# Performance work log

Hardware: AMD Instinct MI355X
Metric: run time of the kernel (lower is better)

## Reference

```python
import jax, jax.numpy as jnp
import numpy as np


def _grad(x, axis):
    """torch.gradient with unit spacing: central diff interior, one-sided edges."""
    def sl(a, b):
        idx = [slice(None)] * x.ndim
        idx[axis] = slice(a, b)
        return x[tuple(idx)]
    left = sl(1, 2) - sl(0, 1)                 # (x[1]-x[0])
    mid = (sl(2, None) - sl(0, -2)) * 0.5      # (x[i+1]-x[i-1])/2
    right = sl(-1, None) - sl(-2, -1)          # (x[-1]-x[-2])
    return jnp.concatenate([left, mid, right], axis=axis)


def _mse0(e):
    return jnp.mean(e * e)  # MSE against zeros


def _phy_loss(V_all, P_all, F_all, Re):
    Vy = V_all[:, :, :, :, 0, :]
    Vx = V_all[:, :, :, :, 1, :]
    Vz = V_all[:, :, :, :, 2, :]
    Fy = F_all[:, :, :, :, 0, :]
    Fx = F_all[:, :, :, :, 1, :]
    Fz = F_all[:, :, :, :, 2, :]
    # first derivatives (dims: 1=y, 2=x, 3=z, 4=t)
    dVydt, dVydy, dVydx, dVydz = _grad(Vy, 4), _grad(Vy, 1), _grad(Vy, 2), _grad(Vy, 3)
    dVxdt, dVxdy, dVxdx, dVxdz = _grad(Vx, 4), _grad(Vx, 1), _grad(Vx, 2), _grad(Vx, 3)
    dVzdt, dVzdy, dVzdx, dVzdz = _grad(Vz, 4), _grad(Vz, 1), _grad(Vz, 2), _grad(Vz, 3)
    dPdx, dPdy, dPdz = _grad(P_all, 2), _grad(P_all, 1), _grad(P_all, 3)
    # second derivatives
    lapVx = _grad(dVxdx, 2) + _grad(dVxdy, 1) + _grad(dVxdz, 3)
    lapVy = _grad(dVydx, 2) + _grad(dVydy, 1) + _grad(dVydz, 3)
    lapVz = _grad(dVzdx, 2) + _grad(dVzdy, 1) + _grad(dVzdz, 3)
    e1 = dVydt + (Vx * dVydx + Vy * dVydy + Vz * dVydz + dPdy) - Re * lapVy + Fy
    e2 = dVxdt + (Vx * dVxdx + Vy * dVxdy + Vz * dVxdz + dPdx) - Re * lapVx + Fx
    e3 = dVzdt + (Vx * dVzdx + Vy * dVzdy + Vz * dVzdz + dPdz) - Re * lapVz + Fz
    e4 = dVxdx + dVydy + dVzdz
    return _mse0(e1) + _mse0(e2) + _mse0(e3) + _mse0(e4)


def _time_loss(C_all, Y_data, X_last):
    Y_last = jnp.concatenate([X_last, Y_data[:, :, :, :, :-1]], axis=4)
    t1 = jnp.mean((Y_last - Y_data) ** 2)
    t2 = jnp.mean((C_all - Y_data) ** 2)
    return jnp.where(jax.lax.stop_gradient(t1) < jax.lax.stop_gradient(t2), t2 - t1, 0.0)


def setup_inputs() -> dict:
    key = jax.random.key(0)
    ks = jax.random.split(key, 9)
    B, S, T = 2, 48, 16
    f = jnp.float32
    return {
        "C_all": jax.random.normal(ks[0], (B, S, S, S, T), f),
        "V_all": jax.random.normal(ks[1], (B, S, S, S, 3, T), f),
        "P_all": jax.random.normal(ks[2], (B, S, S, S, T), f),
        "X_all": jax.random.normal(ks[3], (B, S, S, S, T), f),
        "X1_all": jax.random.normal(ks[4], (B, S, S, S, T), f),
        "F_all": jax.random.normal(ks[5], (B, S, S, S, 3, T), f),
        "Re": jnp.ones((1,), f),
        "X_last": jax.random.normal(ks[6], (B, S, S, S, 1), f),
        "Y_data": jax.random.normal(ks[7], (B, S, S, S, T), f),
        "maskd0": jnp.ones((1,), f),
        "maskd1": jnp.ones((1,), f),
        "maskd2": jnp.ones((1,), f),
    }


def reference(C_all, V_all, P_all, X_all, X1_all, F_all, Re, X_last, Y_data, maskd0, maskd1, maskd2):
    main1 = jnp.mean((X1_all - Y_data) ** 2)
    main2 = jnp.mean((X_all - Y_data) ** 2)
    phy = _phy_loss(V_all, P_all, F_all, Re)
    tl = _time_loss(C_all, Y_data, X_last)
    return (main1, main2, phy, tl)
```

## Files before the change

### kernel.cpp

```cpp
#include <hip/hip_runtime.h>

#define S 48
#define T 16
#define NTOT (2 * S * S * S * T)
#define NBLK (2 * S * S)
#define NSLOT 64

using f4 = __attribute__((ext_vector_type(4))) float;

__device__ __forceinline__ float d1(const float* __restrict__ fc, int i, int N, int stride) {
    int dl = (i > 0) ? -stride : 0;
    int dr = (i < N - 1) ? stride : 0;
    float w = (i > 0 && i < N - 1) ? 0.5f : 1.0f;
    return (fc[dr] - fc[dl]) * w;
}

__device__ __forceinline__ float d2c(const float* __restrict__ fc, int i, int N, int stride) {
    int j0, j1, j2;
    float c0, c1, c2;
    if (i == 0)          { j0 = 0;  j1 = 1;  j2 = 2; c0 = 0.5f;  c1 = -1.0f;  c2 = 0.5f;  }
    else if (i == 1)     { j0 = -1; j1 = 0;  j2 = 2; c0 = 0.5f;  c1 = -0.75f; c2 = 0.25f; }
    else if (i == N - 1) { j0 = -2; j1 = -1; j2 = 0; c0 = 0.5f;  c1 = -1.0f;  c2 = 0.5f;  }
    else if (i == N - 2) { j0 = -2; j1 = 0;  j2 = 1; c0 = 0.25f; c1 = -0.75f; c2 = 0.5f;  }
    else                 { j0 = -2; j1 = 0;  j2 = 2; c0 = 0.25f; c1 = -0.5f;  c2 = 0.25f; }
    return c0 * fc[j0 * stride] + c1 * fc[j1 * stride] + c2 * fc[j2 * stride];
}

__device__ __forceinline__ float d2c_i(const float* __restrict__ fc, float center, int stride) {
    return 0.25f * (fc[-2 * stride] + fc[2 * stride]) - 0.5f * center;
}

__global__ __launch_bounds__(256) void fused_loss(
    const float* __restrict__ Cmat, const float* __restrict__ V,
    const float* __restrict__ P, const float* __restrict__ Xa,
    const float* __restrict__ X1a, const float* __restrict__ F,
    const float* __restrict__ Rep, const float* __restrict__ Xlast,
    const float* __restrict__ Y, float* __restrict__ ws)
{
    const int bidx = blockIdx.x;
    const int x = bidx % S;
    const int y = (bidx / S) % S;
    const int b = bidx / (S * S);
    const int sp0 = ((b * S + y) * S + x) * S;
    const int n0 = sp0 * T;
    const int v0 = sp0 * 48;

    __shared__ float sV[3][S][T];
    __shared__ float sP[S][T];
    __shared__ float sY[S][T];

    const int tid = threadIdx.x;

    for (int j = tid; j < 5 * 192; j += 256) {
        const int a  = j / 192;
        const int r  = j % 192;
        const int z  = r >> 2;
        const int t4 = (r & 3) << 2;
        const float* src;
        float* dst;
        if (a < 3)       { src = V + v0 + z * 48 + a * 16 + t4; dst = &sV[a][z][t4]; }
        else if (a == 3) { src = P + n0 + z * 16 + t4;          dst = &sP[z][t4]; }
        else             { src = Y + n0 + z * 16 + t4;          dst = &sY[z][t4]; }
        *reinterpret_cast<f4*>(dst) = *reinterpret_cast<const f4*>(src);
    }
    __syncthreads();

    const float re = Rep[0];
    const bool xint = (x >= 2 && x < S - 2);
    const bool yint = (y >= 2 && y < S - 2);

    float am1 = 0.f, am2 = 0.f, aphy = 0.f, at1 = 0.f, at2 = 0.f;

    #pragma unroll 1
    for (int i = tid; i < S * T; i += 256) {
        const int z = i >> 4;
        const int t = i & 15;
        const int n = n0 + i;
        const int vb = v0 + z * 48 + t;

        const float yv  = sY[z][t];
        const float dm1 = X1a[n] - yv;
        const float dm2 = Xa[n] - yv;
        am1 += dm1 * dm1;
        am2 += dm2 * dm2;
        const float yprev = (t == 0) ? Xlast[sp0 + z] : sY[z][t - 1];
        const float dt1 = yprev - yv;
        const float dt2 = Cmat[n] - yv;
        at1 += dt1 * dt1;
        at2 += dt2 * dt2;

        const float vy = sV[0][z][t], vx = sV[1][z][t], vz = sV[2][z][t];
        float div;

        {
            const float* c = &sV[0][z][t];
            const float ddt = d1(c, t, T, 1);
            const float ddz = d1(c, z, S, T);
            const float lz  = d2c(c, z, S, T);
            const float* g = V + vb;
            const float ddx = d1(g, x, S, 2304);
            const float ddy = d1(g, y, S, 110592);
            const float lx = xint ? d2c_i(g, vy, 2304)   : d2c(g, x, S, 2304);
            const float ly = yint ? d2c_i(g, vy, 110592) : d2c(g, y, S, 110592);
            const float dPdy = d1(P + n, y, S, 36864);
            const float e1 = ddt + (vx * ddx + vy * ddy + vz * ddz + dPdy)
                             - re * (lz + lx + ly) + F[vb];
            aphy += e1 * e1;
            div = ddy;
        }
        {
            const float* c = &sV[1][z][t];
            const float ddt = d1(c, t, T, 1);
            const float ddz = d1(c, z, S, T);
            const float lz  = d2c(c, z, S, T);
            const float* g = V + vb + 16;
            const float ddx = d1(g, x, S, 2304);
            const float ddy = d1(g, y, S, 110592);
            const float lx = xint ? d2c_i(g, vx, 2304)   : d2c(g, x, S, 2304);
            const float ly = yint ? d2c_i(g, vx, 110592) : d2c(g, y, S, 110592);
            const float dPdx = d1(P + n, x, S, 768);
            const float e2 = ddt + (vx * ddx + vy * ddy + vz * ddz + dPdx)
                             - re * (lz + lx + ly) + F[vb + 16];
            aphy += e2 * e2;
            div += ddx;
        }
        {
            const float* c = &sV[2][z][t];
            const float ddt = d1(c, t, T, 1);
            const float ddz = d1(c, z, S, T);
            const float lz  = d2c(c, z, S, T);
            const float* g = V + vb + 32;
            const float ddx = d1(g, x, S, 2304);
            const float ddy = d1(g, y, S, 110592);
            const float lx = xint ? d2c_i(g, vz, 2304)   : d2c(g, x, S, 2304);
            const float ly = yint ? d2c_i(g, vz, 110592) : d2c(g, y, S, 110592);
            const float dPdz = d1(&sP[z][t], z, S, T);
            const float e3 = ddt + (vx * ddx + vy * ddy + vz * ddz + dPdz)
                             - re * (lz + lx + ly) + F[vb + 32];
            aphy += e3 * e3;
            div += ddz;
            aphy += div * div;
        }
    }

    #pragma unroll
    for (int off = 32; off > 0; off >>= 1) {
        am1  += __shfl_down(am1, off);
        am2  += __shfl_down(am2, off);
        aphy += __shfl_down(aphy, off);
        at1  += __shfl_down(at1, off);
        at2  += __shfl_down(at2, off);
    }
    __shared__ float sred[4][5];
    const int lane = tid & 63;
    const int wv   = tid >> 6;
    if (lane == 0) {
        sred[wv][0] = am1; sred[wv][1] = am2; sred[wv][2] = aphy;
        sred[wv][3] = at1; sred[wv][4] = at2;
    }
    __syncthreads();
    if (tid == 0) {
        float s0 = 0.f, s1 = 0.f, s2 = 0.f, s3 = 0.f, s4 = 0.f;
        #pragma unroll
        for (int w = 0; w < 4; ++w) {
            s0 += sred[w][0]; s1 += sred[w][1]; s2 += sred[w][2];
            s3 += sred[w][3]; s4 += sred[w][4];
        }
        float* slot = ws + (bidx & (NSLOT - 1)) * 16;
        atomicAdd(&slot[0], s0);
        atomicAdd(&slot[1], s1);
        atomicAdd(&slot[2], s2);
        atomicAdd(&slot[3], s3);
        atomicAdd(&slot[4], s4);
    }
}

__global__ void finalize_kernel(const float* __restrict__ ws, float* __restrict__ out) {
    const int l = threadIdx.x;
    float s0 = ws[l * 16 + 0];
    float s1 = ws[l * 16 + 1];
    float s2 = ws[l * 16 + 2];
    float s3 = ws[l * 16 + 3];
    float s4 = ws[l * 16 + 4];
    #pragma unroll
    for (int off = 32; off > 0; off >>= 1) {
        s0 += __shfl_down(s0, off);
        s1 += __shfl_down(s1, off);
        s2 += __shfl_down(s2, off);
        s3 += __shfl_down(s3, off);
        s4 += __shfl_down(s4, off);
    }
    if (l == 0) {
        const float invN = 1.0f / (float)NTOT;
        const float m1  = s0 * invN;
        const float m2  = s1 * invN;
        const float phy = s2 * invN;
        const float t1  = s3 * invN;
        const float t2  = s4 * invN;
        out[0] = m1;
        out[1] = m2;
        out[2] = phy;
        out[3] = (t1 < t2) ? (t2 - t1) : 0.0f;
    }
}

extern "C" void kernel_launch(void* const* d_in, const int* in_sizes, int n_in,
                              void* d_out, int out_size, void* d_ws, size_t ws_size,
                              hipStream_t stream) {
    const float* Cmat  = (const float*)d_in[0];
    const float* V     = (const float*)d_in[1];
    const float* P     = (const float*)d_in[2];
    const float* Xa    = (const float*)d_in[3];
    const float* X1a   = (const float*)d_in[4];
    const float* F     = (const float*)d_in[5];
    const float* Rep   = (const float*)d_in[6];
    const float* Xlast = (const float*)d_in[7];
    const float* Y     = (const float*)d_in[8];

    float* ws  = (float*)d_ws;
    float* out = (float*)d_out;

    hipMemsetAsync(ws, 0, NSLOT * 16 * sizeof(float), stream);
    fused_loss<<<NBLK, 256, 0, stream>>>(Cmat, V, P, Xa, X1a, F, Rep, Xlast, Y, ws);
    finalize_kernel<<<1, 64, 0, stream>>>(ws, out);
}
```

Baseline: 230.0 us.

## Vectorize stencil loss to four time steps per thread with float4 loads

```diff
diff --git a/kernel.cpp b/kernel.cpp
--- a/kernel.cpp
+++ b/kernel.cpp
@@ -4,18 +4,24 @@
 #define T 16
 #define NTOT (2 * S * S * S * T)
 #define NBLK (2 * S * S)
+#define NTHR 192
 #define NSLOT 64
 
 using f4 = __attribute__((ext_vector_type(4))) float;
 
-__device__ __forceinline__ float d1(const float* __restrict__ fc, int i, int N, int stride) {
-    int dl = (i > 0) ? -stride : 0;
-    int dr = (i < N - 1) ? stride : 0;
-    float w = (i > 0 && i < N - 1) ? 0.5f : 1.0f;
-    return (fc[dr] - fc[dl]) * w;
-}
-
-__device__ __forceinline__ float d2c(const float* __restrict__ fc, int i, int N, int stride) {
+__device__ __forceinline__ f4 ld4(const float* __restrict__ p) {
+    return *reinterpret_cast<const f4*>(p);
+}
+__device__ __forceinline__ float dot4(f4 a) { return (a[0] + a[1]) + (a[2] + a[3]); }
+
+__device__ __forceinline__ f4 d1v(const float* __restrict__ fc, int i, int N, int stride) {
+    const int dl = (i > 0) ? -stride : 0;
+    const int dr = (i < N - 1) ? stride : 0;
+    const float w = (i > 0 && i < N - 1) ? 0.5f : 1.0f;
+    return (ld4(fc + dr) - ld4(fc + dl)) * w;
+}
+
+__device__ __forceinline__ f4 d2cv(const float* __restrict__ fc, int i, int N, int stride) {
     int j0, j1, j2;
     float c0, c1, c2;
     if (i == 0)          { j0 = 0;  j1 = 1;  j2 = 2; c0 = 0.5f;  c1 = -1.0f;  c2 = 0.5f;  }
@@ -23,14 +29,21 @@
     else if (i == N - 1) { j0 = -2; j1 = -1; j2 = 0; c0 = 0.5f;  c1 = -1.0f;  c2 = 0.5f;  }
     else if (i == N - 2) { j0 = -2; j1 = 0;  j2 = 1; c0 = 0.25f; c1 = -0.75f; c2 = 0.5f;  }
     else                 { j0 = -2; j1 = 0;  j2 = 2; c0 = 0.25f; c1 = -0.5f;  c2 = 0.25f; }
-    return c0 * fc[j0 * stride] + c1 * fc[j1 * stride] + c2 * fc[j2 * stride];
-}
-
-__device__ __forceinline__ float d2c_i(const float* __restrict__ fc, float center, int stride) {
-    return 0.25f * (fc[-2 * stride] + fc[2 * stride]) - 0.5f * center;
-}
-
-__global__ __launch_bounds__(256) void fused_loss(
+    return c0 * ld4(fc + j0 * stride) + c1 * ld4(fc + j1 * stride) + c2 * ld4(fc + j2 * stride);
+}
+
+__device__ __forceinline__ f4 dtv(const float* __restrict__ row, f4 c, int t4) {
+    const float lf = (t4 > 0)     ? row[-1] : 0.f;
+    const float rt = (t4 < T - 4) ? row[4]  : 0.f;
+    f4 r;
+    r[0] = (t4 == 0)     ? (c[1] - c[0]) : 0.5f * (c[1] - lf);
+    r[1] = 0.5f * (c[2] - c[0]);
+    r[2] = 0.5f * (c[3] - c[1]);
+    r[3] = (t4 == T - 4) ? (c[3] - c[2]) : 0.5f * (rt - c[2]);
+    return r;
+}
+
+__global__ __launch_bounds__(NTHR) void fused_loss(
     const float* __restrict__ Cmat, const float* __restrict__ V,
     const float* __restrict__ P, const float* __restrict__ Xa,
     const float* __restrict__ X1a, const float* __restrict__ F,
@@ -47,122 +60,122 @@
 
     __shared__ float sV[3][S][T];
     __shared__ float sP[S][T];
-    __shared__ float sY[S][T];
 
     const int tid = threadIdx.x;
 
-    for (int j = tid; j < 5 * 192; j += 256) {
+    for (int j = tid; j < 4 * 192; j += NTHR) {
         const int a  = j / 192;
         const int r  = j % 192;
-        const int z  = r >> 2;
-        const int t4 = (r & 3) << 2;
-        const float* src;
-        float* dst;
-        if (a < 3)       { src = V + v0 + z * 48 + a * 16 + t4; dst = &sV[a][z][t4]; }
-        else if (a == 3) { src = P + n0 + z * 16 + t4;          dst = &sP[z][t4]; }
-        else             { src = Y + n0 + z * 16 + t4;          dst = &sY[z][t4]; }
-        *reinterpret_cast<f4*>(dst) = *reinterpret_cast<const f4*>(src);
+        const int zz = r >> 2;
+        const int tt = (r & 3) << 2;
+        const float* src = (a < 3) ? (V + v0 + zz * 48 + a * 16 + tt)
+                                   : (P + n0 + zz * 16 + tt);
+        float* dst = (a < 3) ? &sV[a][zz][tt] : &sP[zz][tt];
+        *reinterpret_cast<f4*>(dst) = ld4(src);
     }
     __syncthreads();
 
     const float re = Rep[0];
-    const bool xint = (x >= 2 && x < S - 2);
-    const bool yint = (y >= 2 && y < S - 2);
-
-    float am1 = 0.f, am2 = 0.f, aphy = 0.f, at1 = 0.f, at2 = 0.f;
-
-    #pragma unroll 1
-    for (int i = tid; i < S * T; i += 256) {
-        const int z = i >> 4;
-        const int t = i & 15;
-        const int n = n0 + i;
-        const int vb = v0 + z * 48 + t;
-
-        const float yv  = sY[z][t];
-        const float dm1 = X1a[n] - yv;
-        const float dm2 = Xa[n] - yv;
-        am1 += dm1 * dm1;
-        am2 += dm2 * dm2;
-        const float yprev = (t == 0) ? Xlast[sp0 + z] : sY[z][t - 1];
-        const float dt1 = yprev - yv;
-        const float dt2 = Cmat[n] - yv;
-        at1 += dt1 * dt1;
-        at2 += dt2 * dt2;
-
-        const float vy = sV[0][z][t], vx = sV[1][z][t], vz = sV[2][z][t];
-        float div;
-
-        {
-            const float* c = &sV[0][z][t];
-            const float ddt = d1(c, t, T, 1);
-            const float ddz = d1(c, z, S, T);
-            const float lz  = d2c(c, z, S, T);
-            const float* g = V + vb;
-            const float ddx = d1(g, x, S, 2304);
-            const float ddy = d1(g, y, S, 110592);
-            const float lx = xint ? d2c_i(g, vy, 2304)   : d2c(g, x, S, 2304);
-            const float ly = yint ? d2c_i(g, vy, 110592) : d2c(g, y, S, 110592);
-            const float dPdy = d1(P + n, y, S, 36864);
-            const float e1 = ddt + (vx * ddx + vy * ddy + vz * ddz + dPdy)
-                             - re * (lz + lx + ly) + F[vb];
-            aphy += e1 * e1;
-            div = ddy;
-        }
-        {
-            const float* c = &sV[1][z][t];
-            const float ddt = d1(c, t, T, 1);
-            const float ddz = d1(c, z, S, T);
-            const float lz  = d2c(c, z, S, T);
-            const float* g = V + vb + 16;
-            const float ddx = d1(g, x, S, 2304);
-            const float ddy = d1(g, y, S, 110592);
-            const float lx = xint ? d2c_i(g, vx, 2304)   : d2c(g, x, S, 2304);
-            const float ly = yint ? d2c_i(g, vx, 110592) : d2c(g, y, S, 110592);
-            const float dPdx = d1(P + n, x, S, 768);
-            const float e2 = ddt + (vx * ddx + vy * ddy + vz * ddz + dPdx)
-                             - re * (lz + lx + ly) + F[vb + 16];
-            aphy += e2 * e2;
-            div += ddx;
-        }
-        {
-            const float* c = &sV[2][z][t];
-            const float ddt = d1(c, t, T, 1);
-            const float ddz = d1(c, z, S, T);
-            const float lz  = d2c(c, z, S, T);
-            const float* g = V + vb + 32;
-            const float ddx = d1(g, x, S, 2304);
-            const float ddy = d1(g, y, S, 110592);
-            const float lx = xint ? d2c_i(g, vz, 2304)   : d2c(g, x, S, 2304);
-            const float ly = yint ? d2c_i(g, vz, 110592) : d2c(g, y, S, 110592);
-            const float dPdz = d1(&sP[z][t], z, S, T);
-            const float e3 = ddt + (vx * ddx + vy * ddy + vz * ddz + dPdz)
-                             - re * (lz + lx + ly) + F[vb + 32];
-            aphy += e3 * e3;
-            div += ddz;
-            aphy += div * div;
-        }
+    const bool xi = (x >= 2 && x < S - 2);
+    const bool yi = (y >= 2 && y < S - 2);
+
+    const int z  = tid >> 2;
+    const int t4 = (tid & 3) << 2;
+    const int n4 = n0 + z * 16 + t4;
+    const int vb = v0 + z * 48 + t4;
+
+    const f4 yv = ld4(Y + n4);
+    f4 dm = ld4(X1a + n4) - yv;  float am1 = dot4(dm * dm);
+    dm = ld4(Xa + n4) - yv;      float am2 = dot4(dm * dm);
+    dm = ld4(Cmat + n4) - yv;    float at2 = dot4(dm * dm);
+    f4 yp;
+    yp[0] = (t4 == 0) ? Xlast[sp0 + z] : Y[n4 - 1];
+    yp[1] = yv[0]; yp[2] = yv[1]; yp[3] = yv[2];
+    dm = yp - yv;                float at1 = dot4(dm * dm);
+
+    const f4 cy = ld4(&sV[0][z][t4]);
+    const f4 cx = ld4(&sV[1][z][t4]);
+    const f4 cz = ld4(&sV[2][z][t4]);
+
+    float sph = 0.f;
+    f4 div;
+
+    {
+        const float* c = &sV[0][z][t4];
+        const f4 ddt = dtv(c, cy, t4);
+        const f4 ddz = d1v(c, z, S, T);
+        const f4 lz  = d2cv(c, z, S, T);
+        const float* g = V + vb;
+        const f4 ddx = d1v(g, x, S, 2304);
+        const f4 ddy = d1v(g, y, S, 110592);
+        const f4 lx = xi ? (0.25f * (ld4(g - 4608)   + ld4(g + 4608))   - 0.5f * cy)
+                         : d2cv(g, x, S, 2304);
+        const f4 ly = yi ? (0.25f * (ld4(g - 221184) + ld4(g + 221184)) - 0.5f * cy)
+                         : d2cv(g, y, S, 110592);
+        const f4 dP = d1v(P + n4, y, S, 36864);
+        const f4 e  = ddt + (cx * ddx + cy * ddy + cz * ddz + dP)
+                      - re * (lz + lx + ly) + ld4(F + vb);
+        sph += dot4(e * e);
+        div = ddy;
+    }
+    {
+        const float* c = &sV[1][z][t4];
+        const f4 ddt = dtv(c, cx, t4);
+        const f4 ddz = d1v(c, z, S, T);
+        const f4 lz  = d2cv(c, z, S, T);
+        const float* g = V + vb + 16;
+        const f4 ddx = d1v(g, x, S, 2304);
+        const f4 ddy = d1v(g, y, S, 110592);
+        const f4 lx = xi ? (0.25f * (ld4(g - 4608)   + ld4(g + 4608))   - 0.5f * cx)
+                         : d2cv(g, x, S, 2304);
+        const f4 ly = yi ? (0.25f * (ld4(g - 221184) + ld4(g + 221184)) - 0.5f * cx)
+                         : d2cv(g, y, S, 110592);
+        const f4 dP = d1v(P + n4, x, S, 768);
+        const f4 e  = ddt + (cx * ddx + cy * ddy + cz * ddz + dP)
+                      - re * (lz + lx + ly) + ld4(F + vb + 16);
+        sph += dot4(e * e);
+        div += ddx;
+    }
+    {
+        const float* c = &sV[2][z][t4];
+        const f4 ddt = dtv(c, cz, t4);
+        const f4 ddz = d1v(c, z, S, T);
+        const f4 lz  = d2cv(c, z, S, T);
+        const float* g = V + vb + 32;
+        const f4 ddx = d1v(g, x, S, 2304);
+        const f4 ddy = d1v(g, y, S, 110592);
+        const f4 lx = xi ? (0.25f * (ld4(g - 4608)   + ld4(g + 4608))   - 0.5f * cz)
+                         : d2cv(g, x, S, 2304);
+        const f4 ly = yi ? (0.25f * (ld4(g - 221184) + ld4(g + 221184)) - 0.5f * cz)
+                         : d2cv(g, y, S, 110592);
+        const f4 dP = d1v(&sP[z][t4], z, S, T);
+        const f4 e  = ddt + (cx * ddx + cy * ddy + cz * ddz + dP)
+                      - re * (lz + lx + ly) + ld4(F + vb + 32);
+        sph += dot4(e * e);
+        div += ddz;
+        sph += dot4(div * div);
     }
 
     #pragma unroll
     for (int off = 32; off > 0; off >>= 1) {
-        am1  += __shfl_down(am1, off);
-        am2  += __shfl_down(am2, off);
-        aphy += __shfl_down(aphy, off);
-        at1  += __shfl_down(at1, off);
-        at2  += __shfl_down(at2, off);
-    }
-    __shared__ float sred[4][5];
+        am1 += __shfl_down(am1, off);
+        am2 += __shfl_down(am2, off);
+        sph += __shfl_down(sph, off);
+        at1 += __shfl_down(at1, off);
+        at2 += __shfl_down(at2, off);
+    }
+    __shared__ float sred[3][5];
     const int lane = tid & 63;
     const int wv   = tid >> 6;
     if (lane == 0) {
-        sred[wv][0] = am1; sred[wv][1] = am2; sred[wv][2] = aphy;
+        sred[wv][0] = am1; sred[wv][1] = am2; sred[wv][2] = sph;
         sred[wv][3] = at1; sred[wv][4] = at2;
     }
     __syncthreads();
     if (tid == 0) {
         float s0 = 0.f, s1 = 0.f, s2 = 0.f, s3 = 0.f, s4 = 0.f;
         #pragma unroll
-        for (int w = 0; w < 4; ++w) {
+        for (int w = 0; w < 3; ++w) {
             s0 += sred[w][0]; s1 += sred[w][1]; s2 += sred[w][2];
             s3 += sred[w][3]; s4 += sred[w][4];
         }
@@ -221,6 +234,6 @@
     float* out = (float*)d_out;
 
     hipMemsetAsync(ws, 0, NSLOT * 16 * sizeof(float), stream);
-    fused_loss<<<NBLK, 256, 0, stream>>>(Cmat, V, P, Xa, X1a, F, Rep, Xlast, Y, ws);
+    fused_loss<<<NBLK, NTHR, 0, stream>>>(Cmat, V, P, Xa, X1a, F, Rep, Xlast, Y, ws);
     finalize_kernel<<<1, 64, 0, stream>>>(ws, out);
 }
```

New measurement: 228.2 us. About the same (-0.8%).
